# Optimization experiments

Measured on AMD Instinct MI355X. Metric: run time of the kernel, lower is better.

Reference implementation:

```python
import jax, jax.numpy as jnp
import numpy as np

N = 8192
F_IN = 256
F_OUT = 128
SLOPE = 0.2
NEG_INF = -9000000000000000.0


def setup_inputs() -> dict:
    key = jax.random.key(0)
    k1, k2, k3, k4, k5 = jax.random.split(key, 5)
    x = jax.random.normal(k1, (N, F_IN), dtype=jnp.float32)
    adj = jax.random.randint(k2, (N, N), 0, 2).astype(jnp.float32)
    W = jax.random.normal(k3, (F_IN, F_OUT), dtype=jnp.float32) * (1.0 / np.sqrt(F_IN))
    a_src = jax.random.normal(k4, (F_OUT,), dtype=jnp.float32) * (1.0 / np.sqrt(F_OUT))
    a_dst = jax.random.normal(k5, (F_OUT,), dtype=jnp.float32) * (1.0 / np.sqrt(F_OUT))
    return {"x": x, "adj": adj, "W": W, "a_src": a_src, "a_dst": a_dst}


def reference(x, adj, W, a_src, a_dst):
    # h: (N, F_OUT)
    h = x @ W
    f_src = h @ a_src  # (N,)
    f_dst = h @ a_dst  # (N,)
    # additive attention scores: (N, N)
    e = f_src[:, None] + f_dst[None, :]
    e = jnp.where(e >= 0, e, SLOPE * e)  # leaky_relu
    e = jnp.where(adj > 0, e, NEG_INF)
    alpha = jax.nn.softmax(e, axis=1)  # (N, N)
    return alpha @ h  # (N, F_OUT)
```

## Files before the change

kernel.cpp:

```cpp
#include <hip/hip_runtime.h>
#include <hip/hip_bf16.h>

#define NN 8192
#define FIN 256
#define FO 128
#define KSPLIT 8
#define JCHUNK (NN / KSPLIT)
#define L2E 1.4426950408889634f

typedef __bf16 bf16x8 __attribute__((ext_vector_type(8)));
typedef __bf16 bf16x2 __attribute__((ext_vector_type(2)));
typedef float  f32x4  __attribute__((ext_vector_type(4)));

__global__ __launch_bounds__(256) void k_proj(
    const float* __restrict__ x, const float* __restrict__ W,
    const float* __restrict__ a_src, const float* __restrict__ a_dst,
    __bf16* __restrict__ Bp, float* __restrict__ f_src, float* __restrict__ f_dst)
{
  __shared__ float xs[16 * FIN];
  __shared__ float fs[16], fd[16];
  const int tid = threadIdx.x;
  const int i0 = blockIdx.x * 16;

  const float4* xg = (const float4*)(x + (size_t)i0 * FIN);
  float4* xs4 = (float4*)xs;
  #pragma unroll
  for (int t = 0; t < 4; t++) xs4[tid + 256 * t] = xg[tid + 256 * t];
  if (tid < 16) { fs[tid] = 0.f; fd[tid] = 0.f; }
  __syncthreads();

  const int cq = tid & 31;
  const int rg = tid >> 5;
  const int c0 = cq * 4;
  const int r0 = rg * 2;
  float acc0[4] = {0.f,0.f,0.f,0.f};
  float acc1[4] = {0.f,0.f,0.f,0.f};
  const float* xr0 = xs + r0 * FIN;
  const float* xr1 = xs + (r0 + 1) * FIN;

  for (int k = 0; k < FIN; k += 4) {
    float4 xa = *(const float4*)(xr0 + k);
    float4 xb = *(const float4*)(xr1 + k);
    #pragma unroll
    for (int kk = 0; kk < 4; kk++) {
      float4 wv = *(const float4*)(W + (size_t)(k + kk) * FO + c0);
      float xav = ((const float*)&xa)[kk];
      float xbv = ((const float*)&xb)[kk];
      acc0[0] += xav * wv.x; acc0[1] += xav * wv.y;
      acc0[2] += xav * wv.z; acc0[3] += xav * wv.w;
      acc1[0] += xbv * wv.x; acc1[1] += xbv * wv.y;
      acc1[2] += xbv * wv.z; acc1[3] += xbv * wv.w;
    }
  }

  float4 as = *(const float4*)(a_src + c0);
  float4 ad = *(const float4*)(a_dst + c0);
  float ps0 = acc0[0]*as.x + acc0[1]*as.y + acc0[2]*as.z + acc0[3]*as.w;
  float ps1 = acc1[0]*as.x + acc1[1]*as.y + acc1[2]*as.z + acc1[3]*as.w;
  float pd0 = acc0[0]*ad.x + acc0[1]*ad.y + acc0[2]*ad.z + acc0[3]*ad.w;
  float pd1 = acc1[0]*ad.x + acc1[1]*ad.y + acc1[2]*ad.z + acc1[3]*ad.w;
  atomicAdd(&fs[r0],     ps0);
  atomicAdd(&fs[r0 + 1], ps1);
  atomicAdd(&fd[r0],     pd0);
  atomicAdd(&fd[r0 + 1], pd1);

  const int j0 = i0 + r0;
  const int kg = j0 >> 5;
  const int q  = (j0 >> 3) & 3;
  const int t0 = j0 & 7;
  #pragma unroll
  for (int c = 0; c < 4; c++) {
    const int n = c0 + c;
    bf16x2 v;
    v[0] = (__bf16)acc0[c];
    v[1] = (__bf16)acc1[c];
    size_t idx = ((size_t)(kg * 8 + (n >> 4)) * 64 + q * 16 + (n & 15)) * 8 + t0;
    *(bf16x2*)(Bp + idx) = v;
  }
  __syncthreads();
  if (tid < 16) { f_src[i0 + tid] = fs[tid]; f_dst[i0 + tid] = fd[tid]; }
}

__global__ __launch_bounds__(256, 4) void k_attn(
    const float* __restrict__ adj, const __bf16* __restrict__ Bp,
    const float* __restrict__ f_src, const float* __restrict__ f_dst,
    float* __restrict__ num, float* __restrict__ lsum)
{
  __shared__ float dls[2 * JCHUNK];
  const int tid = threadIdx.x;
  const int rb = blockIdx.x >> 3;
  const int ks = blockIdx.x & 7;
  const int jbase = ks * JCHUNK;

  for (int t = tid; t < JCHUNK; t += 256) {
    float d = f_dst[jbase + t];
    dls[2 * t]     = d * L2E;
    dls[2 * t + 1] = d * (0.2f * L2E);
  }

  const int wv = tid >> 6;
  const int lane = tid & 63;
  const int m = lane & 15;
  const int q = lane >> 4;
  const int i0 = rb * 64 + wv * 16;
  const float s  = f_src[i0 + m];
  const float s1 = s * L2E;
  const float s2 = s * (0.2f * L2E);
  __syncthreads();

  f32x4 acc[8];
  #pragma unroll
  for (int t = 0; t < 8; t++) acc[t] = (f32x4){0.f, 0.f, 0.f, 0.f};
  float psum = 0.f;

  const float*  adjp = adj + (size_t)(i0 + m) * NN + jbase + q * 8;
  const __bf16* bb   = Bp + (size_t)(ks * (JCHUNK / 32)) * 4096 + lane * 8;

  #pragma unroll 2
  for (int st = 0; st < JCHUNK / 32; st++) {
    const int koff = st * 32;
    float4 a0 = *(const float4*)(adjp + koff);
    float4 a1 = *(const float4*)(adjp + koff + 4);
    const float4* dp = (const float4*)(dls + 2 * (koff + q * 8));
    float4 d0 = dp[0], d1 = dp[1], d2 = dp[2], d3 = dp[3];

    float e0 = __builtin_amdgcn_exp2f(fmaxf(s1 + d0.x, s2 + d0.y));
    float e1 = __builtin_amdgcn_exp2f(fmaxf(s1 + d0.z, s2 + d0.w));
    float e2 = __builtin_amdgcn_exp2f(fmaxf(s1 + d1.x, s2 + d1.y));
    float e3 = __builtin_amdgcn_exp2f(fmaxf(s1 + d1.z, s2 + d1.w));
    float e4 = __builtin_amdgcn_exp2f(fmaxf(s1 + d2.x, s2 + d2.y));
    float e5 = __builtin_amdgcn_exp2f(fmaxf(s1 + d2.z, s2 + d2.w));
    float e6 = __builtin_amdgcn_exp2f(fmaxf(s1 + d3.x, s2 + d3.y));
    float e7 = __builtin_amdgcn_exp2f(fmaxf(s1 + d3.z, s2 + d3.w));
    float p0 = (a0.x > 0.f) ? e0 : 0.f;
    float p1 = (a0.y > 0.f) ? e1 : 0.f;
    float p2 = (a0.z > 0.f) ? e2 : 0.f;
    float p3 = (a0.w > 0.f) ? e3 : 0.f;
    float p4 = (a1.x > 0.f) ? e4 : 0.f;
    float p5 = (a1.y > 0.f) ? e5 : 0.f;
    float p6 = (a1.z > 0.f) ? e6 : 0.f;
    float p7 = (a1.w > 0.f) ? e7 : 0.f;
    psum += ((p0 + p1) + (p2 + p3)) + ((p4 + p5) + (p6 + p7));

    bf16x8 af;
    af[0] = (__bf16)p0; af[1] = (__bf16)p1; af[2] = (__bf16)p2; af[3] = (__bf16)p3;
    af[4] = (__bf16)p4; af[5] = (__bf16)p5; af[6] = (__bf16)p6; af[7] = (__bf16)p7;

    const __bf16* bs = bb + (size_t)st * 4096;
    #pragma unroll
    for (int nt = 0; nt < 8; nt++) {
      bf16x8 bfrag = *(const bf16x8*)(bs + nt * 512);
      acc[nt] = __builtin_amdgcn_mfma_f32_16x16x32_bf16(af, bfrag, acc[nt], 0, 0, 0);
    }
  }

  psum += __shfl_xor(psum, 16);
  psum += __shfl_xor(psum, 32);
  if (lane < 16) atomicAdd(&lsum[i0 + lane], psum);

  #pragma unroll
  for (int nt = 0; nt < 8; nt++) {
    #pragma unroll
    for (int r = 0; r < 4; r++) {
      atomicAdd(&num[(size_t)(i0 + q * 4 + r) * FO + nt * 16 + m], acc[nt][r]);
    }
  }
}

__global__ __launch_bounds__(256) void k_div(
    const float* __restrict__ num, const float* __restrict__ lsum,
    float* __restrict__ out)
{
  int idx = blockIdx.x * 256 + threadIdx.x;
  float4 v = ((const float4*)num)[idx];
  float inv = 1.0f / lsum[idx >> 5];
  float4 o;
  o.x = v.x * inv; o.y = v.y * inv; o.z = v.z * inv; o.w = v.w * inv;
  ((float4*)out)[idx] = o;
}

extern "C" void kernel_launch(void* const* d_in, const int* in_sizes, int n_in,
                              void* d_out, int out_size, void* d_ws, size_t ws_size,
                              hipStream_t stream) {
  const float* x     = (const float*)d_in[0];
  const float* adj   = (const float*)d_in[1];
  const float* W     = (const float*)d_in[2];
  const float* a_src = (const float*)d_in[3];
  const float* a_dst = (const float*)d_in[4];
  float* out = (float*)d_out;

  char* ws = (char*)d_ws;
  __bf16* Bp   = (__bf16*)ws;
  float* f_src = (float*)(ws + 2097152);
  float* f_dst = (float*)(ws + 2097152 + 32768);
  float* num   = (float*)(ws + 2097152 + 65536);
  float* lsum  = (float*)(ws + 2097152 + 65536 + 4194304);

  hipMemsetAsync(num, 0, 4194304 + 32768, stream);
  hipLaunchKernelGGL(k_proj, dim3(512), dim3(256), 0, stream,
                     x, W, a_src, a_dst, Bp, f_src, f_dst);
  hipLaunchKernelGGL(k_attn, dim3(1024), dim3(256), 0, stream,
                     adj, Bp, f_src, f_dst, num, lsum);
  hipLaunchKernelGGL(k_div, dim3(1024), dim3(256), 0, stream,
                     num, lsum, out);
}
```

Baseline: 461.6 us.

## Fuse split-K reduction and normalization into attention kernel via shared-memory accumulation

```diff
diff --git a/kernel.cpp b/kernel.cpp
--- a/kernel.cpp
+++ b/kernel.cpp
@@ -4,9 +4,9 @@
 #define NN 8192
 #define FIN 256
 #define FO 128
-#define KSPLIT 8
-#define JCHUNK (NN / KSPLIT)
+#define JC 1024
 #define L2E 1.4426950408889634f
+#define C2  0.28853900817779268f
 
 typedef __bf16 bf16x8 __attribute__((ext_vector_type(8)));
 typedef __bf16 bf16x2 __attribute__((ext_vector_type(2)));
@@ -81,31 +81,33 @@
   if (tid < 16) { f_src[i0 + tid] = fs[tid]; f_dst[i0 + tid] = fd[tid]; }
 }
 
-__global__ __launch_bounds__(256, 4) void k_attn(
+__global__ __launch_bounds__(512, 4) void k_attn(
     const float* __restrict__ adj, const __bf16* __restrict__ Bp,
     const float* __restrict__ f_src, const float* __restrict__ f_dst,
-    float* __restrict__ num, float* __restrict__ lsum)
+    float* __restrict__ out)
 {
-  __shared__ float dls[2 * JCHUNK];
+  __shared__ float fdls[NN];
+  __shared__ float accbuf[16 * FO];
+  __shared__ float lred[16];
   const int tid = threadIdx.x;
-  const int rb = blockIdx.x >> 3;
-  const int ks = blockIdx.x & 7;
-  const int jbase = ks * JCHUNK;
-
-  for (int t = tid; t < JCHUNK; t += 256) {
-    float d = f_dst[jbase + t];
-    dls[2 * t]     = d * L2E;
-    dls[2 * t + 1] = d * (0.2f * L2E);
-  }
+  const int i0 = blockIdx.x * 16;
+
+  {
+    const float4* src = (const float4*)f_dst;
+    float4* dst = (float4*)fdls;
+    #pragma unroll
+    for (int t = 0; t < 4; t++) dst[tid + 512 * t] = src[tid + 512 * t];
+  }
+  ((float4*)accbuf)[tid] = (float4){0.f, 0.f, 0.f, 0.f};
+  if (tid < 16) lred[tid] = 0.f;
 
   const int wv = tid >> 6;
   const int lane = tid & 63;
   const int m = lane & 15;
   const int q = lane >> 4;
-  const int i0 = rb * 64 + wv * 16;
   const float s  = f_src[i0 + m];
   const float s1 = s * L2E;
-  const float s2 = s * (0.2f * L2E);
+  const float s2 = s * 0.2f * L2E;
   __syncthreads();
 
   f32x4 acc[8];
@@ -113,70 +115,85 @@
   for (int t = 0; t < 8; t++) acc[t] = (f32x4){0.f, 0.f, 0.f, 0.f};
   float psum = 0.f;
 
-  const float*  adjp = adj + (size_t)(i0 + m) * NN + jbase + q * 8;
-  const __bf16* bb   = Bp + (size_t)(ks * (JCHUNK / 32)) * 4096 + lane * 8;
-
-  #pragma unroll 2
-  for (int st = 0; st < JCHUNK / 32; st++) {
-    const int koff = st * 32;
-    float4 a0 = *(const float4*)(adjp + koff);
-    float4 a1 = *(const float4*)(adjp + koff + 4);
-    const float4* dp = (const float4*)(dls + 2 * (koff + q * 8));
-    float4 d0 = dp[0], d1 = dp[1], d2 = dp[2], d3 = dp[3];
-
-    float e0 = __builtin_amdgcn_exp2f(fmaxf(s1 + d0.x, s2 + d0.y));
-    float e1 = __builtin_amdgcn_exp2f(fmaxf(s1 + d0.z, s2 + d0.w));
-    float e2 = __builtin_amdgcn_exp2f(fmaxf(s1 + d1.x, s2 + d1.y));
-    float e3 = __builtin_amdgcn_exp2f(fmaxf(s1 + d1.z, s2 + d1.w));
-    float e4 = __builtin_amdgcn_exp2f(fmaxf(s1 + d2.x, s2 + d2.y));
-    float e5 = __builtin_amdgcn_exp2f(fmaxf(s1 + d2.z, s2 + d2.w));
-    float e6 = __builtin_amdgcn_exp2f(fmaxf(s1 + d3.x, s2 + d3.y));
-    float e7 = __builtin_amdgcn_exp2f(fmaxf(s1 + d3.z, s2 + d3.w));
-    float p0 = (a0.x > 0.f) ? e0 : 0.f;
-    float p1 = (a0.y > 0.f) ? e1 : 0.f;
-    float p2 = (a0.z > 0.f) ? e2 : 0.f;
-    float p3 = (a0.w > 0.f) ? e3 : 0.f;
-    float p4 = (a1.x > 0.f) ? e4 : 0.f;
-    float p5 = (a1.y > 0.f) ? e5 : 0.f;
-    float p6 = (a1.z > 0.f) ? e6 : 0.f;
-    float p7 = (a1.w > 0.f) ? e7 : 0.f;
-    psum += ((p0 + p1) + (p2 + p3)) + ((p4 + p5) + (p6 + p7));
-
-    bf16x8 af;
-    af[0] = (__bf16)p0; af[1] = (__bf16)p1; af[2] = (__bf16)p2; af[3] = (__bf16)p3;
-    af[4] = (__bf16)p4; af[5] = (__bf16)p5; af[6] = (__bf16)p6; af[7] = (__bf16)p7;
-
-    const __bf16* bs = bb + (size_t)st * 4096;
-    #pragma unroll
-    for (int nt = 0; nt < 8; nt++) {
-      bf16x8 bfrag = *(const bf16x8*)(bs + nt * 512);
-      acc[nt] = __builtin_amdgcn_mfma_f32_16x16x32_bf16(af, bfrag, acc[nt], 0, 0, 0);
-    }
-  }
+  const float*  adjp  = adj + (size_t)(i0 + m) * NN + wv * JC + q * 8;
+  const __bf16* bb    = Bp + (size_t)wv * 32 * 4096 + lane * 8;
+  const float*  dbase = fdls + wv * JC + q * 8;
+
+  float4 pa0[4], pa1[4];
+  #pragma unroll
+  for (int p = 0; p < 4; p++) {
+    pa0[p] = *(const float4*)(adjp + p * 32);
+    pa1[p] = *(const float4*)(adjp + p * 32 + 4);
+  }
+
+#define ATTN_STEP(stc, u, PREFETCH)                                          \
+  {                                                                          \
+    float4 a0 = pa0[u], a1 = pa1[u];                                         \
+    if (PREFETCH) {                                                          \
+      pa0[u] = *(const float4*)(adjp + ((stc) + 4) * 32);                    \
+      pa1[u] = *(const float4*)(adjp + ((stc) + 4) * 32 + 4);                \
+    }                                                                        \
+    const float4* dp = (const float4*)(dbase + (stc) * 32);                  \
+    float4 d0 = dp[0], d1 = dp[1];                                           \
+    float e0 = __builtin_amdgcn_exp2f(fmaxf(fmaf(d0.x, L2E, s1), fmaf(d0.x, C2, s2))); \
+    float e1 = __builtin_amdgcn_exp2f(fmaxf(fmaf(d0.y, L2E, s1), fmaf(d0.y, C2, s2))); \
+    float e2 = __builtin_amdgcn_exp2f(fmaxf(fmaf(d0.z, L2E, s1), fmaf(d0.z, C2, s2))); \
+    float e3 = __builtin_amdgcn_exp2f(fmaxf(fmaf(d0.w, L2E, s1), fmaf(d0.w, C2, s2))); \
+    float e4 = __builtin_amdgcn_exp2f(fmaxf(fmaf(d1.x, L2E, s1), fmaf(d1.x, C2, s2))); \
+    float e5 = __builtin_amdgcn_exp2f(fmaxf(fmaf(d1.y, L2E, s1), fmaf(d1.y, C2, s2))); \
+    float e6 = __builtin_amdgcn_exp2f(fmaxf(fmaf(d1.z, L2E, s1), fmaf(d1.z, C2, s2))); \
+    float e7 = __builtin_amdgcn_exp2f(fmaxf(fmaf(d1.w, L2E, s1), fmaf(d1.w, C2, s2))); \
+    float p0 = (a0.x > 0.f) ? e0 : 0.f;                                      \
+    float p1 = (a0.y > 0.f) ? e1 : 0.f;                                      \
+    float p2 = (a0.z > 0.f) ? e2 : 0.f;                                      \
+    float p3 = (a0.w > 0.f) ? e3 : 0.f;                                      \
+    float p4 = (a1.x > 0.f) ? e4 : 0.f;                                      \
+    float p5 = (a1.y > 0.f) ? e5 : 0.f;                                      \
+    float p6 = (a1.z > 0.f) ? e6 : 0.f;                                      \
+    float p7 = (a1.w > 0.f) ? e7 : 0.f;                                      \
+    psum += ((p0 + p1) + (p2 + p3)) + ((p4 + p5) + (p6 + p7));               \
+    bf16x8 af;                                                               \
+    af[0] = (__bf16)p0; af[1] = (__bf16)p1; af[2] = (__bf16)p2; af[3] = (__bf16)p3; \
+    af[4] = (__bf16)p4; af[5] = (__bf16)p5; af[6] = (__bf16)p6; af[7] = (__bf16)p7; \
+    const __bf16* bs = bb + (size_t)(stc) * 4096;                            \
+    _Pragma("unroll")                                                        \
+    for (int nt = 0; nt < 8; nt++) {                                         \
+      bf16x8 bfrag = *(const bf16x8*)(bs + nt * 512);                        \
+      acc[nt] = __builtin_amdgcn_mfma_f32_16x16x32_bf16(af, bfrag, acc[nt], 0, 0, 0); \
+    }                                                                        \
+  }
+
+  for (int st = 0; st < 28; st += 4) {
+    ATTN_STEP(st + 0, 0, true)
+    ATTN_STEP(st + 1, 1, true)
+    ATTN_STEP(st + 2, 2, true)
+    ATTN_STEP(st + 3, 3, true)
+  }
+  ATTN_STEP(28, 0, false)
+  ATTN_STEP(29, 1, false)
+  ATTN_STEP(30, 2, false)
+  ATTN_STEP(31, 3, false)
+#undef ATTN_STEP
 
   psum += __shfl_xor(psum, 16);
   psum += __shfl_xor(psum, 32);
-  if (lane < 16) atomicAdd(&lsum[i0 + lane], psum);
+  if (lane < 16) atomicAdd(&lred[lane], psum);
 
   #pragma unroll
   for (int nt = 0; nt < 8; nt++) {
     #pragma unroll
     for (int r = 0; r < 4; r++) {
-      atomicAdd(&num[(size_t)(i0 + q * 4 + r) * FO + nt * 16 + m], acc[nt][r]);
+      atomicAdd(&accbuf[(q * 4 + r) * FO + nt * 16 + m], acc[nt][r]);
     }
   }
-}
-
-__global__ __launch_bounds__(256) void k_div(
-    const float* __restrict__ num, const float* __restrict__ lsum,
-    float* __restrict__ out)
-{
-  int idx = blockIdx.x * 256 + threadIdx.x;
-  float4 v = ((const float4*)num)[idx];
-  float inv = 1.0f / lsum[idx >> 5];
+  __syncthreads();
+
+  const int row = tid >> 5;
+  const float inv = 1.0f / lred[row];
+  float4 v = ((const float4*)accbuf)[tid];
   float4 o;
   o.x = v.x * inv; o.y = v.y * inv; o.z = v.z * inv; o.w = v.w * inv;
-  ((float4*)out)[idx] = o;
+  ((float4*)(out + (size_t)i0 * FO))[tid] = o;
 }
 
 extern "C" void kernel_launch(void* const* d_in, const int* in_sizes, int n_in,
@@ -193,14 +210,9 @@
   __bf16* Bp   = (__bf16*)ws;
   float* f_src = (float*)(ws + 2097152);
   float* f_dst = (float*)(ws + 2097152 + 32768);
-  float* num   = (float*)(ws + 2097152 + 65536);
-  float* lsum  = (float*)(ws + 2097152 + 65536 + 4194304);
-
-  hipMemsetAsync(num, 0, 4194304 + 32768, stream);
+
   hipLaunchKernelGGL(k_proj, dim3(512), dim3(256), 0, stream,
                      x, W, a_src, a_dst, Bp, f_src, f_dst);
-  hipLaunchKernelGGL(k_attn, dim3(1024), dim3(256), 0, stream,
-                     adj, Bp, f_src, f_dst, num, lsum);
-  hipLaunchKernelGGL(k_div, dim3(1024), dim3(256), 0, stream,
-                     num, lsum, out);
+  hipLaunchKernelGGL(k_attn, dim3(512), dim3(512), 0, stream,
+                     adj, Bp, f_src, f_dst, out);
 }
```

After: 539.8 us. 1.17x slower.

## Stage attention probabilities in LDS tile and compute row sums via MFMA

Applied to the files above, without the earlier changes.

```diff
diff --git a/kernel.cpp b/kernel.cpp
--- a/kernel.cpp
+++ b/kernel.cpp
@@ -4,11 +4,16 @@
 #define NN 8192
 #define FIN 256
 #define FO 128
-#define KSPLIT 8
+#define KSPLIT 4
 #define JCHUNK (NN / KSPLIT)
+#define KSTEP 256
+#define NSTEP (JCHUNK / KSTEP)
+#define PSTRIDE 280
 #define L2E 1.4426950408889634f
+#define C2  0.28853900817779268f
 
 typedef __bf16 bf16x8 __attribute__((ext_vector_type(8)));
+typedef __bf16 bf16x4 __attribute__((ext_vector_type(4)));
 typedef __bf16 bf16x2 __attribute__((ext_vector_type(2)));
 typedef float  f32x4  __attribute__((ext_vector_type(4)));
 
@@ -86,84 +91,111 @@
     const float* __restrict__ f_src, const float* __restrict__ f_dst,
     float* __restrict__ num, float* __restrict__ lsum)
 {
-  __shared__ float dls[2 * JCHUNK];
+  __shared__ float fdls[JCHUNK];
+  __shared__ __align__(16) __bf16 ptile[2 * 16 * PSTRIDE];
   const int tid = threadIdx.x;
-  const int rb = blockIdx.x >> 3;
-  const int ks = blockIdx.x & 7;
+  const int rg = blockIdx.x >> 2;
+  const int ks = blockIdx.x & 3;
+  const int i0 = rg * 32;
   const int jbase = ks * JCHUNK;
 
-  for (int t = tid; t < JCHUNK; t += 256) {
-    float d = f_dst[jbase + t];
-    dls[2 * t]     = d * L2E;
-    dls[2 * t + 1] = d * (0.2f * L2E);
-  }
-
-  const int wv = tid >> 6;
+  {
+    const float4* s = (const float4*)(f_dst + jbase);
+    float4* d4 = (float4*)fdls;
+    d4[tid] = s[tid];
+    d4[tid + 256] = s[tid + 256];
+  }
+
+  const int w = tid >> 6;
   const int lane = tid & 63;
   const int m = lane & 15;
   const int q = lane >> 4;
-  const int i0 = rb * 64 + wv * 16;
-  const float s  = f_src[i0 + m];
-  const float s1 = s * L2E;
-  const float s2 = s * (0.2f * L2E);
+  const int mt = w & 1;
+  const int h = w >> 1;
+
+  float fsv[8];
+  #pragma unroll
+  for (int it = 0; it < 8; it++) fsv[it] = f_src[i0 + it * 4 + w];
+
+  f32x4 acc[8];
+  #pragma unroll
+  for (int t = 0; t < 8; t++) acc[t] = (f32x4){0.f, 0.f, 0.f, 0.f};
+  f32x4 accl = (f32x4){0.f, 0.f, 0.f, 0.f};
+  bf16x8 ones;
+  #pragma unroll
+  for (int t = 0; t < 8; t++) ones[t] = (__bf16)1.0f;
+
+  const float* adjb = adj + (size_t)i0 * NN + jbase + lane * 4;
+  const __bf16* prd = ptile + mt * (16 * PSTRIDE) + m * PSTRIDE + q * 8;
+
   __syncthreads();
 
-  f32x4 acc[8];
-  #pragma unroll
-  for (int t = 0; t < 8; t++) acc[t] = (f32x4){0.f, 0.f, 0.f, 0.f};
-  float psum = 0.f;
-
-  const float*  adjp = adj + (size_t)(i0 + m) * NN + jbase + q * 8;
-  const __bf16* bb   = Bp + (size_t)(ks * (JCHUNK / 32)) * 4096 + lane * 8;
-
-  #pragma unroll 2
-  for (int st = 0; st < JCHUNK / 32; st++) {
-    const int koff = st * 32;
-    float4 a0 = *(const float4*)(adjp + koff);
-    float4 a1 = *(const float4*)(adjp + koff + 4);
-    const float4* dp = (const float4*)(dls + 2 * (koff + q * 8));
-    float4 d0 = dp[0], d1 = dp[1], d2 = dp[2], d3 = dp[3];
-
-    float e0 = __builtin_amdgcn_exp2f(fmaxf(s1 + d0.x, s2 + d0.y));
-    float e1 = __builtin_amdgcn_exp2f(fmaxf(s1 + d0.z, s2 + d0.w));
-    float e2 = __builtin_amdgcn_exp2f(fmaxf(s1 + d1.x, s2 + d1.y));
-    float e3 = __builtin_amdgcn_exp2f(fmaxf(s1 + d1.z, s2 + d1.w));
-    float e4 = __builtin_amdgcn_exp2f(fmaxf(s1 + d2.x, s2 + d2.y));
-    float e5 = __builtin_amdgcn_exp2f(fmaxf(s1 + d2.z, s2 + d2.w));
-    float e6 = __builtin_amdgcn_exp2f(fmaxf(s1 + d3.x, s2 + d3.y));
-    float e7 = __builtin_amdgcn_exp2f(fmaxf(s1 + d3.z, s2 + d3.w));
-    float p0 = (a0.x > 0.f) ? e0 : 0.f;
-    float p1 = (a0.y > 0.f) ? e1 : 0.f;
-    float p2 = (a0.z > 0.f) ? e2 : 0.f;
-    float p3 = (a0.w > 0.f) ? e3 : 0.f;
-    float p4 = (a1.x > 0.f) ? e4 : 0.f;
-    float p5 = (a1.y > 0.f) ? e5 : 0.f;
-    float p6 = (a1.z > 0.f) ? e6 : 0.f;
-    float p7 = (a1.w > 0.f) ? e7 : 0.f;
-    psum += ((p0 + p1) + (p2 + p3)) + ((p4 + p5) + (p6 + p7));
-
-    bf16x8 af;
-    af[0] = (__bf16)p0; af[1] = (__bf16)p1; af[2] = (__bf16)p2; af[3] = (__bf16)p3;
-    af[4] = (__bf16)p4; af[5] = (__bf16)p5; af[6] = (__bf16)p6; af[7] = (__bf16)p7;
-
-    const __bf16* bs = bb + (size_t)st * 4096;
-    #pragma unroll
-    for (int nt = 0; nt < 8; nt++) {
-      bf16x8 bfrag = *(const bf16x8*)(bs + nt * 512);
-      acc[nt] = __builtin_amdgcn_mfma_f32_16x16x32_bf16(af, bfrag, acc[nt], 0, 0, 0);
-    }
-  }
-
-  psum += __shfl_xor(psum, 16);
-  psum += __shfl_xor(psum, 32);
-  if (lane < 16) atomicAdd(&lsum[i0 + lane], psum);
-
+  float4 av[8];
+  #pragma unroll
+  for (int it = 0; it < 8; it++)
+    av[it] = *(const float4*)(adjb + (size_t)(it * 4 + w) * NN);
+
+  for (int step = 0; step < NSTEP; step++) {
+    float4 d = *(const float4*)(fdls + step * KSTEP + lane * 4);
+    float4 dl1, dl2;
+    dl1.x = d.x * L2E; dl1.y = d.y * L2E; dl1.z = d.z * L2E; dl1.w = d.w * L2E;
+    dl2.x = d.x * C2;  dl2.y = d.y * C2;  dl2.z = d.z * C2;  dl2.w = d.w * C2;
+
+    if (step) __syncthreads();
+
+    #pragma unroll
+    for (int it = 0; it < 8; it++) {
+      const int r = it * 4 + w;
+      const float s1 = fsv[it] * L2E;
+      const float s2 = fsv[it] * (0.2f * L2E);
+      float4 a = av[it];
+      float e0 = __builtin_amdgcn_exp2f(fmaxf(dl1.x + s1, dl2.x + s2));
+      float e1 = __builtin_amdgcn_exp2f(fmaxf(dl1.y + s1, dl2.y + s2));
+      float e2 = __builtin_amdgcn_exp2f(fmaxf(dl1.z + s1, dl2.z + s2));
+      float e3 = __builtin_amdgcn_exp2f(fmaxf(dl1.w + s1, dl2.w + s2));
+      float p0 = (a.x > 0.f) ? e0 : 0.f;
+      float p1 = (a.y > 0.f) ? e1 : 0.f;
+      float p2 = (a.z > 0.f) ? e2 : 0.f;
+      float p3 = (a.w > 0.f) ? e3 : 0.f;
+      bf16x4 pv;
+      pv[0] = (__bf16)p0; pv[1] = (__bf16)p1;
+      pv[2] = (__bf16)p2; pv[3] = (__bf16)p3;
+      *(bf16x4*)(ptile + (r >> 4) * (16 * PSTRIDE) + (r & 15) * PSTRIDE + lane * 4) = pv;
+    }
+
+    if (step + 1 < NSTEP) {
+      #pragma unroll
+      for (int it = 0; it < 8; it++)
+        av[it] = *(const float4*)(adjb + (size_t)(it * 4 + w) * NN + (step + 1) * KSTEP);
+    }
+    __syncthreads();
+
+    const int kgbase = (jbase >> 5) + step * 8;
+    #pragma unroll
+    for (int kk = 0; kk < 4; kk++) {
+      const int kg_w = h * 4 + kk;
+      bf16x8 af = *(const bf16x8*)(prd + kg_w * 32);
+      const __bf16* bsrc = Bp + (size_t)(kgbase + kg_w) * 8 * 512 + lane * 8;
+      #pragma unroll
+      for (int nt = 0; nt < 8; nt++) {
+        bf16x8 bfrag = *(const bf16x8*)(bsrc + nt * 512);
+        acc[nt] = __builtin_amdgcn_mfma_f32_16x16x32_bf16(af, bfrag, acc[nt], 0, 0, 0);
+      }
+      accl = __builtin_amdgcn_mfma_f32_16x16x32_bf16(af, ones, accl, 0, 0, 0);
+    }
+  }
+
+  const int rb0 = i0 + mt * 16 + q * 4;
   #pragma unroll
   for (int nt = 0; nt < 8; nt++) {
     #pragma unroll
     for (int r = 0; r < 4; r++) {
-      atomicAdd(&num[(size_t)(i0 + q * 4 + r) * FO + nt * 16 + m], acc[nt][r]);
-    }
+      atomicAdd(&num[(size_t)(rb0 + r) * FO + nt * 16 + m], acc[nt][r]);
+    }
+  }
+  if (m == 0) {
+    #pragma unroll
+    for (int r = 0; r < 4; r++) atomicAdd(&lsum[rb0 + r], accl[r]);
   }
 }
 
```

Result: no change. 465.8 us (+0.9%).

## Factor exp of leaky-relu scores into per-row and per-column exponentials, prefetch adj

Applied to the files above, without the earlier changes.

```diff
diff --git a/kernel.cpp b/kernel.cpp
--- a/kernel.cpp
+++ b/kernel.cpp
@@ -7,6 +7,7 @@
 #define KSPLIT 8
 #define JCHUNK (NN / KSPLIT)
 #define L2E 1.4426950408889634f
+#define C2  0.28853900817779268f
 
 typedef __bf16 bf16x8 __attribute__((ext_vector_type(8)));
 typedef __bf16 bf16x2 __attribute__((ext_vector_type(2)));
@@ -86,72 +87,88 @@
     const float* __restrict__ f_src, const float* __restrict__ f_dst,
     float* __restrict__ num, float* __restrict__ lsum)
 {
-  __shared__ float dls[2 * JCHUNK];
+  __shared__ float G1[JCHUNK];
+  __shared__ float G2[JCHUNK];
   const int tid = threadIdx.x;
   const int rb = blockIdx.x >> 3;
   const int ks = blockIdx.x & 7;
   const int jbase = ks * JCHUNK;
 
-  for (int t = tid; t < JCHUNK; t += 256) {
-    float d = f_dst[jbase + t];
-    dls[2 * t]     = d * L2E;
-    dls[2 * t + 1] = d * (0.2f * L2E);
-  }
-
-  const int wv = tid >> 6;
+  #pragma unroll
+  for (int t = 0; t < 4; t++) {
+    int j = tid + t * 256;
+    float d = f_dst[jbase + j];
+    G1[j] = __builtin_amdgcn_exp2f(d * L2E);
+    G2[j] = __builtin_amdgcn_exp2f(d * C2);
+  }
+
+  const int w = tid >> 6;
   const int lane = tid & 63;
   const int m = lane & 15;
   const int q = lane >> 4;
-  const int i0 = rb * 64 + wv * 16;
+  const int i0 = rb * 64 + w * 16;
   const float s  = f_src[i0 + m];
-  const float s1 = s * L2E;
-  const float s2 = s * (0.2f * L2E);
-  __syncthreads();
+  const float F1 = __builtin_amdgcn_exp2f(s * L2E);
+  const float F2 = __builtin_amdgcn_exp2f(s * C2);
 
   f32x4 acc[8];
   #pragma unroll
   for (int t = 0; t < 8; t++) acc[t] = (f32x4){0.f, 0.f, 0.f, 0.f};
   float psum = 0.f;
 
-  const float*  adjp = adj + (size_t)(i0 + m) * NN + jbase + q * 8;
-  const __bf16* bb   = Bp + (size_t)(ks * (JCHUNK / 32)) * 4096 + lane * 8;
+  const float* adjp = adj + (size_t)(i0 + m) * NN + jbase + q * 8;
+  const float* g1p = G1 + q * 8;
+  const float* g2p = G2 + q * 8;
+  const __bf16* bb = Bp + (size_t)(jbase >> 5) * 4096 + lane * 8;
+
+  __syncthreads();
+
+  float4 cur0 = *(const float4*)(adjp + 0);
+  float4 cur1 = *(const float4*)(adjp + 4);
+  float4 cur2 = *(const float4*)(adjp + 32);
+  float4 cur3 = *(const float4*)(adjp + 36);
 
   #pragma unroll 2
-  for (int st = 0; st < JCHUNK / 32; st++) {
-    const int koff = st * 32;
-    float4 a0 = *(const float4*)(adjp + koff);
-    float4 a1 = *(const float4*)(adjp + koff + 4);
-    const float4* dp = (const float4*)(dls + 2 * (koff + q * 8));
-    float4 d0 = dp[0], d1 = dp[1], d2 = dp[2], d3 = dp[3];
-
-    float e0 = __builtin_amdgcn_exp2f(fmaxf(s1 + d0.x, s2 + d0.y));
-    float e1 = __builtin_amdgcn_exp2f(fmaxf(s1 + d0.z, s2 + d0.w));
-    float e2 = __builtin_amdgcn_exp2f(fmaxf(s1 + d1.x, s2 + d1.y));
-    float e3 = __builtin_amdgcn_exp2f(fmaxf(s1 + d1.z, s2 + d1.w));
-    float e4 = __builtin_amdgcn_exp2f(fmaxf(s1 + d2.x, s2 + d2.y));
-    float e5 = __builtin_amdgcn_exp2f(fmaxf(s1 + d2.z, s2 + d2.w));
-    float e6 = __builtin_amdgcn_exp2f(fmaxf(s1 + d3.x, s2 + d3.y));
-    float e7 = __builtin_amdgcn_exp2f(fmaxf(s1 + d3.z, s2 + d3.w));
-    float p0 = (a0.x > 0.f) ? e0 : 0.f;
-    float p1 = (a0.y > 0.f) ? e1 : 0.f;
-    float p2 = (a0.z > 0.f) ? e2 : 0.f;
-    float p3 = (a0.w > 0.f) ? e3 : 0.f;
-    float p4 = (a1.x > 0.f) ? e4 : 0.f;
-    float p5 = (a1.y > 0.f) ? e5 : 0.f;
-    float p6 = (a1.z > 0.f) ? e6 : 0.f;
-    float p7 = (a1.w > 0.f) ? e7 : 0.f;
-    psum += ((p0 + p1) + (p2 + p3)) + ((p4 + p5) + (p6 + p7));
-
-    bf16x8 af;
-    af[0] = (__bf16)p0; af[1] = (__bf16)p1; af[2] = (__bf16)p2; af[3] = (__bf16)p3;
-    af[4] = (__bf16)p4; af[5] = (__bf16)p5; af[6] = (__bf16)p6; af[7] = (__bf16)p7;
-
-    const __bf16* bs = bb + (size_t)st * 4096;
+  for (int st = 0; st < 16; ++st) {
+    float4 nxt0, nxt1, nxt2, nxt3;
+    if (st < 15) {
+      const float* ap = adjp + (st + 1) * 64;
+      nxt0 = *(const float4*)(ap + 0);
+      nxt1 = *(const float4*)(ap + 4);
+      nxt2 = *(const float4*)(ap + 32);
+      nxt3 = *(const float4*)(ap + 36);
+    }
     #pragma unroll
-    for (int nt = 0; nt < 8; nt++) {
-      bf16x8 bfrag = *(const bf16x8*)(bs + nt * 512);
-      acc[nt] = __builtin_amdgcn_mfma_f32_16x16x32_bf16(af, bfrag, acc[nt], 0, 0, 0);
-    }
+    for (int g = 0; g < 2; ++g) {
+      const int ko = st * 64 + g * 32;
+      float4 a0 = g ? cur2 : cur0;
+      float4 a1 = g ? cur3 : cur1;
+      float4 u0 = *(const float4*)(g1p + ko);
+      float4 u1 = *(const float4*)(g1p + ko + 4);
+      float4 v0 = *(const float4*)(g2p + ko);
+      float4 v1 = *(const float4*)(g2p + ko + 4);
+      float p0 = (a0.x > 0.f) ? fmaxf(F1 * u0.x, F2 * v0.x) : 0.f;
+      float p1 = (a0.y > 0.f) ? fmaxf(F1 * u0.y, F2 * v0.y) : 0.f;
+      float p2 = (a0.z > 0.f) ? fmaxf(F1 * u0.z, F2 * v0.z) : 0.f;
+      float p3 = (a0.w > 0.f) ? fmaxf(F1 * u0.w, F2 * v0.w) : 0.f;
+      float p4 = (a1.x > 0.f) ? fmaxf(F1 * u1.x, F2 * v1.x) : 0.f;
+      float p5 = (a1.y > 0.f) ? fmaxf(F1 * u1.y, F2 * v1.y) : 0.f;
+      float p6 = (a1.z > 0.f) ? fmaxf(F1 * u1.z, F2 * v1.z) : 0.f;
+      float p7 = (a1.w > 0.f) ? fmaxf(F1 * u1.w, F2 * v1.w) : 0.f;
+      psum += ((p0 + p1) + (p2 + p3)) + ((p4 + p5) + (p6 + p7));
+
+      bf16x8 af;
+      af[0] = (__bf16)p0; af[1] = (__bf16)p1; af[2] = (__bf16)p2; af[3] = (__bf16)p3;
+      af[4] = (__bf16)p4; af[5] = (__bf16)p5; af[6] = (__bf16)p6; af[7] = (__bf16)p7;
+
+      const __bf16* bs = bb + (size_t)(st * 2 + g) * 4096;
+      #pragma unroll
+      for (int nt = 0; nt < 8; nt++) {
+        bf16x8 bfrag = *(const bf16x8*)(bs + nt * 512);
+        acc[nt] = __builtin_amdgcn_mfma_f32_16x16x32_bf16(af, bfrag, acc[nt], 0, 0, 0);
+      }
+    }
+    if (st < 15) { cur0 = nxt0; cur1 = nxt1; cur2 = nxt2; cur3 = nxt3; }
   }
 
   psum += __shfl_xor(psum, 16);
```

New measurement: 451.3 us. 1.02x faster.
